# Kernel optimization log

Measured on AMD Instinct MI355X. Metric: run time of the kernel, lower is better.

Reference implementation:

```python
import jax, jax.numpy as jnp
from jax import lax
import numpy as np

# Fixed 3x3 kernels (PyTorch Conv2d = cross-correlation; lax conv is also cross-correlation, no flip)
GAUSS = jnp.array([[0.0625, 0.125, 0.0625], [0.125, 0.25, 0.125], [0.0625, 0.125, 0.0625]], jnp.float32)
SOBEL_X = jnp.array([[-1., -2., -1.], [0., 0., 0.], [1., 2., 1.]], jnp.float32)
SOBEL_Y = jnp.array([[-1., 0., 1.], [-2., 0., 2.], [-1., 0., 1.]], jnp.float32)
PREWITT_X = jnp.array([[1., 1., 1.], [0., 0., 0.], [-1., -1., -1.]], jnp.float32)
PREWITT_Y = jnp.array([[-1., 0., 1.], [-1., 0., 1.], [-1., 0., 1.]], jnp.float32)
ROBERTS_X = jnp.array([[-1., 0., 0.], [0., 1., 0.], [0., 0., 0.]], jnp.float32)
ROBERTS_Y = jnp.array([[0., -1., 0.], [1., 0., 0.], [0., 0., 0.]], jnp.float32)
LAPLACE = jnp.array([[2., 0., 2.], [0., -8., 0.], [2., 0., 2.]], jnp.float32)


def conv3x3_reflect(x, k):
    # x: [B,1,H,W]; reflect pad by 1 then VALID conv (matches padding='same', padding_mode='reflect')
    xp = jnp.pad(x, ((0, 0), (0, 0), (1, 1), (1, 1)), mode='reflect')
    return lax.conv_general_dilated(xp, k[None, None], (1, 1), 'VALID',
                                    dimension_numbers=('NCHW', 'OIHW', 'NCHW'))


def edge_response(x, k):
    # clip(|conv(x)|, 0, 255).round()  (jnp.round = round-half-even, same as torch)
    return jnp.round(jnp.clip(jnp.abs(conv3x3_reflect(x, k)), 0.0, 255.0))


def add_weighted(a, b):
    # AddWeighted(a, 0.5, b, 0.5, 0.0)
    return jnp.round(0.5 * a + 0.5 * b)


def setup_inputs() -> dict:
    key = jax.random.key(0)
    pan = jax.random.uniform(key, (2, 1, 2048, 2048), dtype=jnp.float32)
    return {"pan": pan}


def reference(pan):
    pan_lp = conv3x3_reflect(pan, GAUSS)
    norm = jnp.max(pan_lp, axis=(1, 2, 3), keepdims=True)  # [B,1,1,1]
    pan_lp = pan_lp * 255.0 / norm
    scale = norm / 255.0

    sobel = add_weighted(edge_response(pan_lp, SOBEL_X), edge_response(pan_lp, SOBEL_Y)) * scale

    pan_lp_f = jnp.floor(pan_lp)  # pan_lp // 1.0
    prewitt = add_weighted(edge_response(pan_lp_f, PREWITT_X), edge_response(pan_lp_f, PREWITT_Y)) * scale
    roberts = add_weighted(edge_response(pan_lp_f, ROBERTS_X), edge_response(pan_lp_f, ROBERTS_Y)) * scale
    laplacian = edge_response(pan_lp_f, LAPLACE) * scale

    # forward differences with replicate (edge) padding on left / top
    pan_pad_x = jnp.pad(pan, ((0, 0), (0, 0), (0, 0), (1, 0)), mode='edge')
    pan_pad_y = jnp.pad(pan, ((0, 0), (0, 0), (1, 0), (0, 0)), mode='edge')
    diff_x = pan_pad_x[:, :, :, 1:] - pan_pad_x[:, :, :, :-1]
    diff_y = pan_pad_y[:, :, 1:, :] - pan_pad_y[:, :, :-1, :]

    return jnp.concatenate([diff_y, diff_x, roberts, prewitt, sobel, laplacian], axis=1)
```

## Files before the change

kernel.cpp:

```cpp
#include <hip/hip_runtime.h>

#define HH 2048
#define WW 2048
#define NB 2
#define FEPS 5e-4f

#define BX 32
#define BY 8
#define SPH (BY + 4)
#define SPW (BX + 4)
#define SPP (SPW + 1)
#define SSH (BY + 2)
#define SSW (BX + 2)
#define SSP (SSW + 1)

__device__ __forceinline__ int refl(int i, int n) {
    if (i < 0) return -i;
    if (i >= n) return 2 * n - 2 - i;
    return i;
}

__device__ __forceinline__ float fastrcp(float x) {
#if __has_builtin(__builtin_amdgcn_rcpf)
    return __builtin_amdgcn_rcpf(x);
#else
    return 1.0f / x;
#endif
}

__device__ __forceinline__ float gauss9_f64(float p00, float p01, float p02,
                                            float p10, float p11, float p12,
                                            float p20, float p21, float p22) {
    const double a = 0.0625 * ((double)p00 + (double)p02 + (double)p20 + (double)p22)
                   + 0.125  * ((double)p01 + (double)p10 + (double)p12 + (double)p21)
                   + 0.25   * (double)p11;
    return (float)a;
}

__global__ void init_norm_kernel(unsigned int* nb) {
    if (threadIdx.x < NB) nb[threadIdx.x] = 0u;
}

__global__ __launch_bounds__(256) void gauss_max_kernel(const float* __restrict__ pan,
                                                        unsigned int* __restrict__ norm_bits) {
    const int b = blockIdx.y;
    const float* __restrict__ img = pan + (size_t)b * HH * WW;
    float lmax = 0.0f;
    const int npix = HH * WW;
    for (int p = blockIdx.x * blockDim.x + threadIdx.x; p < npix; p += gridDim.x * blockDim.x) {
        const int i = p >> 11;
        const int j = p & (WW - 1);
        const int im = refl(i - 1, HH), ip = refl(i + 1, HH);
        const int jm = refl(j - 1, WW), jp = refl(j + 1, WW);
        const float g = gauss9_f64(img[im * WW + jm], img[im * WW + j], img[im * WW + jp],
                                   img[i  * WW + jm], img[i  * WW + j], img[i  * WW + jp],
                                   img[ip * WW + jm], img[ip * WW + j], img[ip * WW + jp]);
        lmax = fmaxf(lmax, g);
    }
    #pragma unroll
    for (int off = 32; off > 0; off >>= 1)
        lmax = fmaxf(lmax, __shfl_down(lmax, off, 64));
    __shared__ float smax[4];
    const int lane = threadIdx.x & 63, wid = threadIdx.x >> 6;
    if (lane == 0) smax[wid] = lmax;
    __syncthreads();
    if (threadIdx.x == 0) {
        const float m = fmaxf(fmaxf(smax[0], smax[1]), fmaxf(smax[2], smax[3]));
        atomicMax(norm_bits + b, __float_as_uint(m));
    }
}

__device__ __forceinline__ void epilogue(const float s[3][3], float scale,
                                         float pc, float pup, float pleft,
                                         int i, int j, int b, float* __restrict__ out) {
    float f[3][3];
    #pragma unroll
    for (int di = 0; di < 3; ++di)
        #pragma unroll
        for (int dj = 0; dj < 3; ++dj)
            f[di][dj] = floorf(s[di][dj]);

    const float sx = (s[2][0] + 2.0f * s[2][1] + s[2][2])
                   - (s[0][0] + 2.0f * s[0][1] + s[0][2]);
    const float sy = (s[0][2] + 2.0f * s[1][2] + s[2][2])
                   - (s[0][0] + 2.0f * s[1][0] + s[2][0]);
    const float ex = rintf(fminf(fabsf(sx), 255.0f));
    const float ey = rintf(fminf(fabsf(sy), 255.0f));
    const float sob = rintf(0.5f * ex + 0.5f * ey);

    const float px = (f[0][0] + f[0][1] + f[0][2]) - (f[2][0] + f[2][1] + f[2][2]);
    const float py = (f[0][2] + f[1][2] + f[2][2]) - (f[0][0] + f[1][0] + f[2][0]);
    const float epx = rintf(fminf(fabsf(px), 255.0f));
    const float epy = rintf(fminf(fabsf(py), 255.0f));
    const float prew = rintf(0.5f * epx + 0.5f * epy);

    const float rx = f[1][1] - f[0][0];
    const float ry = f[1][0] - f[0][1];
    const float erx = rintf(fminf(fabsf(rx), 255.0f));
    const float ery = rintf(fminf(fabsf(ry), 255.0f));
    const float rob = rintf(0.5f * erx + 0.5f * ery);

    float el;
    {
        const float fr11 = s[1][1] - f[1][1];
        const int um = (fr11 < FEPS) || (fr11 > 1.0f - FEPS);
        const float m0 = (um && fr11 < FEPS) ? f[1][1] - 1.0f : f[1][1];

        float S0 = 0.0f; int nu = 0;
        {
            const float fr = s[0][0] - f[0][0];
            const int u = (fr < FEPS) || (fr > 1.0f - FEPS);
            S0 += (u && fr < FEPS) ? f[0][0] - 1.0f : f[0][0]; nu += u;
        }
        {
            const float fr = s[0][2] - f[0][2];
            const int u = (fr < FEPS) || (fr > 1.0f - FEPS);
            S0 += (u && fr < FEPS) ? f[0][2] - 1.0f : f[0][2]; nu += u;
        }
        {
            const float fr = s[2][0] - f[2][0];
            const int u = (fr < FEPS) || (fr > 1.0f - FEPS);
            S0 += (u && fr < FEPS) ? f[2][0] - 1.0f : f[2][0]; nu += u;
        }
        {
            const float fr = s[2][2] - f[2][2];
            const int u = (fr < FEPS) || (fr > 1.0f - FEPS);
            S0 += (u && fr < FEPS) ? f[2][2] - 1.0f : f[2][2]; nu += u;
        }

        if ((um | nu) == 0) {
            const float tt = 2.0f * S0 - 8.0f * m0;
            el = rintf(fminf(fabsf(tt), 255.0f));
        } else {
            float Lmin = 1e30f, Lmax = -1e30f;
            for (int mm = 0; mm <= um; ++mm) {
                const float mval = m0 + (float)mm;
                for (int jj = 0; jj <= nu; ++jj) {
                    const float tt = 2.0f * (S0 + (float)jj) - 8.0f * mval;
                    const float L = rintf(fminf(fabsf(tt), 255.0f));
                    Lmin = fminf(Lmin, L);
                    Lmax = fmaxf(Lmax, L);
                }
            }
            el = 0.5f * (Lmin + Lmax);
        }
    }

    const float dy = (i > 0) ? __fsub_rn(pc, pup) : 0.0f;
    const float dx = (j > 0) ? __fsub_rn(pc, pleft) : 0.0f;

    const size_t plane = (size_t)HH * WW;
    const size_t base = ((size_t)(b * 6) * HH + i) * WW + j;
    out[base]             = dy;
    out[base + plane]     = dx;
    out[base + 2 * plane] = __fmul_rn(rob,  scale);
    out[base + 3 * plane] = __fmul_rn(prew, scale);
    out[base + 4 * plane] = __fmul_rn(sob,  scale);
    out[base + 5 * plane] = __fmul_rn(el,   scale);
}

__global__ __launch_bounds__(256) void fused_kernel(const float* __restrict__ pan,
                                                    const unsigned int* __restrict__ norm_bits,
                                                    float* __restrict__ out) {
    __shared__ float sp[SPH][SPP];
    __shared__ float ss[SSH][SSP];

    const int b  = blockIdx.z;
    const int bi = blockIdx.y * BY;
    const int bj = blockIdx.x * BX;
    const float* __restrict__ img = pan + (size_t)b * HH * WW;
    const int tx = threadIdx.x, ty = threadIdx.y;
    const int tid = ty * BX + tx;

    const float norm = __uint_as_float(norm_bits[b]);

    const bool interior = (blockIdx.x >= 1) & (blockIdx.x <= (WW / BX) - 2) &
                          (blockIdx.y >= 1) & (blockIdx.y <= (HH / BY) - 2);
    if (interior) {
        const int r = tid >> 4;
        const int q = tid & 15;
        if (r < SPH && q < 10) {
            const float* rowp = img + (size_t)(bi - 2 + r) * WW + (bj - 4 + 4 * q);
            const float4 v = *(const float4*)rowp;
            const int c0 = 4 * q - 2;
            if (q == 0) {
                sp[r][0] = v.z; sp[r][1] = v.w;
            } else if (q == 9) {
                sp[r][34] = v.x; sp[r][35] = v.y;
            } else {
                sp[r][c0] = v.x; sp[r][c0 + 1] = v.y;
                sp[r][c0 + 2] = v.z; sp[r][c0 + 3] = v.w;
            }
        }
    } else {
        for (int idx = tid; idx < SPH * SPW; idx += 256) {
            const int rr = idx / SPW, cc = idx % SPW;
            sp[rr][cc] = img[refl(bi - 2 + rr, HH) * WW + refl(bj - 2 + cc, WW)];
        }
    }
    __syncthreads();

    const float rnorm = fastrcp(norm);
    for (int idx = tid; idx < SSH * SSW; idx += 256) {
        const int r = idx / SSW, c = idx % SSW;
        const float g = gauss9_f64(sp[r][c],   sp[r][c+1],   sp[r][c+2],
                                   sp[r+1][c], sp[r+1][c+1], sp[r+1][c+2],
                                   sp[r+2][c], sp[r+2][c+1], sp[r+2][c+2]);
        ss[r][c] = __fmul_rn(__fmul_rn(g, 255.0f), rnorm);
    }
    __syncthreads();

    const float scale = __fmul_rn(norm, (1.0f / 255.0f));
    const int i = bi + ty, j = bj + tx;

    float s[3][3];
    #pragma unroll
    for (int di = 0; di < 3; ++di)
        #pragma unroll
        for (int dj = 0; dj < 3; ++dj)
            s[di][dj] = ss[ty + di][tx + dj];

    const float pc    = sp[ty + 2][tx + 2];
    const float pup   = sp[ty + 1][tx + 2];
    const float pleft = sp[ty + 2][tx + 1];

    epilogue(s, scale, pc, pup, pleft, i, j, b, out);
}

extern "C" void kernel_launch(void* const* d_in, const int* in_sizes, int n_in,
                              void* d_out, int out_size, void* d_ws, size_t ws_size,
                              hipStream_t stream) {
    const float* pan = (const float*)d_in[0];
    float* out = (float*)d_out;
    unsigned int* norm_bits = (unsigned int*)d_ws;

    hipLaunchKernelGGL(init_norm_kernel, dim3(1), dim3(64), 0, stream, norm_bits);
    hipLaunchKernelGGL(gauss_max_kernel, dim3(1024, NB), dim3(256), 0, stream, pan, norm_bits);
    dim3 grid(WW / BX, HH / BY, NB);
    dim3 block(BX, BY);
    hipLaunchKernelGGL(fused_kernel, grid, block, 0, stream, pan, norm_bits, out);
}
```

Measured before the change: 85.01 us.

## Restructure gauss-max pass to one row per block with vectorized 8-pixel strips

The max-reduction pass now assigns one image row to each block, and each thread covers eight consecutive pixels. Each thread loads its three-row neighbourhood once with float4 loads plus halo scalars, and reuses the values across the eight Gaussian evaluations instead of issuing nine scalar gathers per pixel. Row indices are interleaved across blocks, and the grid grows to one block per row. This cuts load instructions and index arithmetic in the pre-pass, in exchange for more blocks and more atomics.

```diff
diff --git a/kernel.cpp b/kernel.cpp
--- a/kernel.cpp
+++ b/kernel.cpp
@@ -44,17 +44,39 @@
 __global__ __launch_bounds__(256) void gauss_max_kernel(const float* __restrict__ pan,
                                                         unsigned int* __restrict__ norm_bits) {
     const int b = blockIdx.y;
+    const int bid = blockIdx.x;
+    const int i = (bid & 7) * 256 + (bid >> 3);
     const float* __restrict__ img = pan + (size_t)b * HH * WW;
+    const int t = threadIdx.x;
+    const int j0 = t * 8;
+    const int im = refl(i - 1, HH), ip = refl(i + 1, HH);
+    const float* __restrict__ r0 = img + (size_t)im * WW;
+    const float* __restrict__ r1 = img + (size_t)i  * WW;
+    const float* __restrict__ r2 = img + (size_t)ip * WW;
+
+    float c0[10], c1[10], c2[10];
+    {
+        const float4 B0 = *(const float4*)(r0 + j0);
+        const float4 C0 = *(const float4*)(r0 + j0 + 4);
+        const float4 B1 = *(const float4*)(r1 + j0);
+        const float4 C1 = *(const float4*)(r1 + j0 + 4);
+        const float4 B2 = *(const float4*)(r2 + j0);
+        const float4 C2 = *(const float4*)(r2 + j0 + 4);
+        c0[1]=B0.x; c0[2]=B0.y; c0[3]=B0.z; c0[4]=B0.w; c0[5]=C0.x; c0[6]=C0.y; c0[7]=C0.z; c0[8]=C0.w;
+        c1[1]=B1.x; c1[2]=B1.y; c1[3]=B1.z; c1[4]=B1.w; c1[5]=C1.x; c1[6]=C1.y; c1[7]=C1.z; c1[8]=C1.w;
+        c2[1]=B2.x; c2[2]=B2.y; c2[3]=B2.z; c2[4]=B2.w; c2[5]=C2.x; c2[6]=C2.y; c2[7]=C2.z; c2[8]=C2.w;
+        if (t == 0) { c0[0] = B0.y; c1[0] = B1.y; c2[0] = B2.y; }
+        else        { c0[0] = r0[j0-1]; c1[0] = r1[j0-1]; c2[0] = r2[j0-1]; }
+        if (t == 255) { c0[9] = C0.z; c1[9] = C1.z; c2[9] = C2.z; }
+        else          { c0[9] = r0[j0+8]; c1[9] = r1[j0+8]; c2[9] = r2[j0+8]; }
+    }
+
     float lmax = 0.0f;
-    const int npix = HH * WW;
-    for (int p = blockIdx.x * blockDim.x + threadIdx.x; p < npix; p += gridDim.x * blockDim.x) {
-        const int i = p >> 11;
-        const int j = p & (WW - 1);
-        const int im = refl(i - 1, HH), ip = refl(i + 1, HH);
-        const int jm = refl(j - 1, WW), jp = refl(j + 1, WW);
-        const float g = gauss9_f64(img[im * WW + jm], img[im * WW + j], img[im * WW + jp],
-                                   img[i  * WW + jm], img[i  * WW + j], img[i  * WW + jp],
-                                   img[ip * WW + jm], img[ip * WW + j], img[ip * WW + jp]);
+    #pragma unroll
+    for (int k = 0; k < 8; ++k) {
+        const float g = gauss9_f64(c0[k], c0[k+1], c0[k+2],
+                                   c1[k], c1[k+1], c1[k+2],
+                                   c2[k], c2[k+1], c2[k+2]);
         lmax = fmaxf(lmax, g);
     }
     #pragma unroll
@@ -235,7 +257,7 @@
     unsigned int* norm_bits = (unsigned int*)d_ws;
 
     hipLaunchKernelGGL(init_norm_kernel, dim3(1), dim3(64), 0, stream, norm_bits);
-    hipLaunchKernelGGL(gauss_max_kernel, dim3(1024, NB), dim3(256), 0, stream, pan, norm_bits);
+    hipLaunchKernelGGL(gauss_max_kernel, dim3(HH, NB), dim3(256), 0, stream, pan, norm_bits);
     dim3 grid(WW / BX, HH / BY, NB);
     dim3 block(BX, BY);
     hipLaunchKernelGGL(fused_kernel, grid, block, 0, stream, pan, norm_bits, out);
```

New measurement: 104.3 us. +22.7%, slower.
